# Optimization experiments

Hardware: AMD Instinct MI355X
Metric: run time of the kernel (lower is better)

## Reference

```python
import jax, jax.numpy as jnp
import numpy as np

# NOTE: ffn(in, out, capacity=1, activation) is assumed to be a single Linear(in, out)
# followed by the activation (ReLU). Dropout is identity in eval mode.

B, M, H, Eh = 16, 128, 256, 128

def setup_inputs() -> dict:
    key = jax.random.key(0)
    ks = jax.random.split(key, 12)
    s = lambda n: 1.0 / np.sqrt(n)
    return {
        "X": jax.random.normal(ks[0], (B, M, H), jnp.float32),
        "E": jax.random.normal(ks[1], (B, M, M, Eh), jnp.float32),
        "A": jax.random.uniform(ks[2], (B, M, M), jnp.float32),
        "eps": jnp.zeros((1,), jnp.float32),
        "We": jax.random.normal(ks[3], (Eh, Eh), jnp.float32) * s(Eh),
        "be": jnp.zeros((Eh,), jnp.float32),
        "Wr": jax.random.normal(ks[4], (H + Eh, H), jnp.float32) * s(H + Eh),
        "br": jnp.zeros((H,), jnp.float32),
        "W0": jax.random.normal(ks[5], (H, H), jnp.float32) * s(H),
        "b0": jnp.zeros((H,), jnp.float32),
        "W1": jax.random.normal(ks[6], (H, H), jnp.float32) * s(H),
        "b1": jnp.zeros((H,), jnp.float32),
    }

def reference(X, E, A, eps, We, be, Wr, br, W0, b0, W1, b1):
    act = jax.nn.relu
    # edge_mapper: ffn(e, e, capacity=1) -> Linear + activation
    Em = act(jnp.einsum('bije,ef->bijf', E, We) + be)          # (b,m,m,e)
    # msg[b,j,:] = sum_i A[b,i,j] * cat(X[b,i,:], Em[b,i,j,:])
    # fused: avoids materializing the (b,m,m,h+e) intermediate
    msg_x = jnp.einsum('bij,bih->bjh', A, X)                   # (b,m,h)
    msg_e = jnp.einsum('bij,bije->bje', A, Em)                 # (b,m,e)
    msg = jnp.concatenate([msg_x, msg_e], axis=-1)             # (b,m,h+e)
    Xs = (1.0 + eps) * X
    out = Xs + act(jnp.einsum('bmc,ch->bmh', msg, Wr) + br)    # residual_mapping
    out = jnp.einsum('bmh,hk->bmk', out, W0) + b0
    out = act(out)  # dropout p is identity in eval mode
    out = jnp.einsum('bmh,hk->bmk', out, W1) + b1
    out = act(out)
    return out
```

## Files before the change

### kernel.cpp

```cpp
#include <hip/hip_runtime.h>

typedef float        f32x4  __attribute__((ext_vector_type(4)));
typedef __bf16       bf16x8 __attribute__((ext_vector_type(8)));
typedef unsigned int u32x4  __attribute__((ext_vector_type(4)));
typedef unsigned short u16;

#define MFMA16(a,b,c) __builtin_amdgcn_mfma_f32_16x16x32_bf16((a),(b),(c),0,0,0)

typedef __attribute__((address_space(3))) unsigned int       as3_u32;
typedef __attribute__((address_space(1))) const unsigned int as1_u32;
__device__ __forceinline__ void gld16(const float* g, float* l) {
    __builtin_amdgcn_global_load_lds((as1_u32*)g, (as3_u32*)l, 16, 0, 0);
}

__device__ __forceinline__ unsigned bf_rnd(float x) {
    unsigned u = __float_as_uint(x);
    return (u + 0x7FFFu + ((u >> 16) & 1u)) & 0xFFFF0000u;
}
__device__ __forceinline__ void split_bf(float x, unsigned &h, unsigned &l) {
    unsigned hr = bf_rnd(x);
    h = hr >> 16;
    float lo = x - __uint_as_float(hr);
    l = bf_rnd(lo) >> 16;
}
__device__ __forceinline__ void split8q(const f32x4 a, const f32x4 b, bf16x8 &hv, bf16x8 &lv) {
    u32x4 hp, lp;
    #pragma unroll
    for (int i = 0; i < 2; ++i) {
        float x0 = (i ? b : a)[0], x1 = (i ? b : a)[1], x2 = (i ? b : a)[2], x3 = (i ? b : a)[3];
        unsigned h0 = __float_as_uint(x0) & 0xFFFF0000u;
        unsigned h1 = __float_as_uint(x1) & 0xFFFF0000u;
        unsigned h2 = __float_as_uint(x2) & 0xFFFF0000u;
        unsigned h3 = __float_as_uint(x3) & 0xFFFF0000u;
        unsigned l0 = bf_rnd(x0 - __uint_as_float(h0));
        unsigned l1 = bf_rnd(x1 - __uint_as_float(h1));
        unsigned l2 = bf_rnd(x2 - __uint_as_float(h2));
        unsigned l3 = bf_rnd(x3 - __uint_as_float(h3));
        hp[i*2+0] = (h0 >> 16) | h1;  lp[i*2+0] = (l0 >> 16) | l1;
        hp[i*2+1] = (h2 >> 16) | h3;  lp[i*2+1] = (l2 >> 16) | l3;
    }
    hv = __builtin_bit_cast(bf16x8, hp);
    lv = __builtin_bit_cast(bf16x8, lp);
}
__device__ __forceinline__ bf16x8 ld16(const u16* p) {
    return __builtin_bit_cast(bf16x8, *(const u32x4*)p);
}

__global__ __launch_bounds__(256) void k_prep(
    const float* __restrict__ We, const float* __restrict__ Wr,
    const float* __restrict__ W0, const float* __restrict__ W1,
    u16* __restrict__ WeTh, u16* __restrict__ WeTl,
    u16* __restrict__ WrTh, u16* __restrict__ WrTl,
    u16* __restrict__ W0Th, u16* __restrict__ W0Tl,
    u16* __restrict__ W1Th, u16* __restrict__ W1Tl)
{
    int t = blockIdx.x * 256 + threadIdx.x;
    float v; u16 *dh, *dl; int dst;
    if (t < 16384) {
        int f = t & 127, e = t >> 7;
        v = We[e*128 + f]; dst = f*128 + e; dh = WeTh; dl = WeTl;
    } else if (t < 16384 + 98304) {
        int u = t - 16384; int h = u & 255, k = u >> 8;
        v = Wr[k*256 + h]; dst = h*384 + k; dh = WrTh; dl = WrTl;
    } else if (t < 16384 + 98304 + 65536) {
        int u = t - 16384 - 98304; int h = u & 255, k = u >> 8;
        v = W0[k*256 + h]; dst = h*256 + k; dh = W0Th; dl = W0Tl;
    } else {
        int u = t - 16384 - 98304 - 65536; int h = u & 255, k = u >> 8;
        v = W1[k*256 + h]; dst = h*256 + k; dh = W1Th; dl = W1Tl;
    }
    unsigned hh, ll; split_bf(v, hh, ll);
    dh[dst] = (u16)hh; dl[dst] = (u16)ll;
}

__device__ __forceinline__ void stage_slab(const float* __restrict__ Eslab,
                                           float* buf, int tid) {
    const int w = tid >> 6, l = tid & 63;
    #pragma unroll
    for (int r = 0; r < 8; ++r) {
        const int q   = (r << 2) + w;
        const int row = (q << 1) + (l >> 5);
        const int cof = (((l & 31) ^ (row & 7)) << 4);
        gld16(Eslab + row*128 + (cof >> 2), buf + (q << 8));
    }
}

__global__ __launch_bounds__(256) __attribute__((amdgpu_waves_per_eu(2, 2)))
void k_edge(
    const float* __restrict__ E, const float* __restrict__ A,
    const u16* __restrict__ WeTh, const u16* __restrict__ WeTl,
    const float* __restrict__ be, float* __restrict__ part)
{
    __shared__ __align__(16) float sE[2][64*128];

    const int tid  = threadIdx.x;
    const int lane = tid & 63;
    const int wv   = tid >> 6;
    const int lrow = lane & 15;
    const int lk   = lane >> 4;
    const int wm   = (wv >> 1) << 5;
    const int wn   = (wv & 1)  << 6;
    const int bid  = blockIdx.x;
    const int jh   = bid & 1;
    const int c    = (bid >> 1) & 15;
    const int b    = bid >> 5;
    const int i0   = c << 3;
    const int j0   = jh << 6;

    bf16x8 wh[4][4], wl[4][4];
    #pragma unroll
    for (int n = 0; n < 4; ++n)
        #pragma unroll
        for (int k = 0; k < 4; ++k) {
            const int off = (wn + n*16 + lrow)*128 + k*32 + lk*8;
            wh[n][k] = ld16(WeTh + off);
            wl[n][k] = ld16(WeTl + off);
        }
    float ber[4];
    #pragma unroll
    for (int n = 0; n < 4; ++n) ber[n] = be[wn + n*16 + lrow];

    const float* Eb = E + ((size_t)((b*128 + i0)*128 + j0)) * 128;
    stage_slab(Eb, sE[0], tid);

    f32x4 P[2][4] = {};

    for (int s = 0; s < 8; ++s) {
        __syncthreads();
        if (s < 7)
            stage_slab(Eb + (size_t)(s+1)*16384, sE[(s+1) & 1], tid);

        const char* buf = (const char*)sE[s & 1];
        f32x4 em[2][4] = {};
        #pragma unroll
        for (int k = 0; k < 4; ++k) {
            #pragma unroll
            for (int m = 0; m < 2; ++m) {
                const int jr = wm + m*16 + lrow;
                const int cb = k*128 + lk*32;
                const int sw = (jr & 7) << 4;
                const f32x4 e0 = *(const f32x4*)(buf + jr*512 + ((cb +  0) ^ sw));
                const f32x4 e1 = *(const f32x4*)(buf + jr*512 + ((cb + 16) ^ sw));
                bf16x8 eh, el; split8q(e0, e1, eh, el);
                #pragma unroll
                for (int n = 0; n < 4; ++n) {
                    em[m][n] = MFMA16(eh, wh[n][k], em[m][n]);
                    em[m][n] = MFMA16(eh, wl[n][k], em[m][n]);
                    em[m][n] = MFMA16(el, wh[n][k], em[m][n]);
                }
            }
        }

        const float* Arow = A + (size_t)(b*128 + i0 + s)*128 + j0;
        #pragma unroll
        for (int m = 0; m < 2; ++m) {
            const f32x4 a4 = *(const f32x4*)(Arow + wm + m*16 + lk*4);
            #pragma unroll
            for (int n = 0; n < 4; ++n)
                #pragma unroll
                for (int r = 0; r < 4; ++r) {
                    float v = fmaxf(em[m][n][r] + ber[n], 0.0f);
                    P[m][n][r] += a4[r] * v;
                }
        }
    }

    float* op = part + (size_t)bid * 8192;
    #pragma unroll
    for (int m = 0; m < 2; ++m)
        #pragma unroll
        for (int r = 0; r < 4; ++r) {
            const int j = wm + m*16 + lk*4 + r;
            #pragma unroll
            for (int n = 0; n < 4; ++n)
                op[j*128 + wn + n*16 + lrow] = P[m][n][r];
        }
}

__global__ __launch_bounds__(256) void k_msg(
    const float* __restrict__ A, const float* __restrict__ X,
    const float* __restrict__ part,
    u16* __restrict__ msg_h, u16* __restrict__ msg_l)
{
    const int bid = blockIdx.x;
    const int tid = threadIdx.x;
    __shared__ float sAt[128*8];

    if (bid < 256) {
        const int b = bid >> 4, jt = bid & 15;
        #pragma unroll
        for (int q = 0; q < 4; ++q) {
            const int e   = (q << 8) + tid;
            const int row = jt*8 + (e >> 7);
            const int f   = e & 127;
            const int jhh = row >> 6, rl = row & 63;
            const float* p = part + ((size_t)(b*32 + jhh))*8192 + rl*128 + f;
            float ssum = 0.f;
            #pragma unroll
            for (int cc = 0; cc < 16; ++cc) ssum += p[(size_t)cc*16384];
            unsigned hh, ll; split_bf(ssum, hh, ll);
            const size_t o = (size_t)(b*128 + row)*384 + 256 + f;
            msg_h[o] = (u16)hh; msg_l[o] = (u16)ll;
        }
    } else {
        const int idx = bid - 256;
        const int b = idx >> 4, jt = idx & 15, j0 = jt << 3;
        #pragma unroll
        for (int q = 0; q < 4; ++q) {
            const int e = tid + q*256;
            sAt[e] = A[(size_t)(b*128 + (e >> 3))*128 + j0 + (e & 7)];
        }
        __syncthreads();
        const int h = tid;
        float acc[8] = {};
        const float* Xb = X + (size_t)b*32768 + h;
        #pragma unroll 2
        for (int i = 0; i < 128; ++i) {
            const float x  = Xb[(size_t)i*256];
            const f32x4 a0 = *(const f32x4*)(sAt + i*8);
            const f32x4 a1 = *(const f32x4*)(sAt + i*8 + 4);
            acc[0] += a0[0]*x; acc[1] += a0[1]*x; acc[2] += a0[2]*x; acc[3] += a0[3]*x;
            acc[4] += a1[0]*x; acc[5] += a1[1]*x; acc[6] += a1[2]*x; acc[7] += a1[3]*x;
        }
        #pragma unroll
        for (int jj = 0; jj < 8; ++jj) {
            unsigned hh, ll; split_bf(acc[jj], hh, ll);
            const size_t o = (size_t)(b*128 + j0 + jj)*384 + h;
            msg_h[o] = (u16)hh; msg_l[o] = (u16)ll;
        }
    }
}

template<int KT, bool RES, bool F32OUT>
__global__ __launch_bounds__(256) void k_tail(
    const u16* __restrict__ Ah, const u16* __restrict__ Al,
    const u16* __restrict__ Bh, const u16* __restrict__ Bl,
    const float* __restrict__ bias, const float* __restrict__ res,
    const float* __restrict__ epsp,
    float* __restrict__ outf, u16* __restrict__ oh, u16* __restrict__ ol)
{
    const int tid  = threadIdx.x;
    const int lane = tid & 63;
    const int wid  = tid >> 6;
    const int lrow = lane & 15;
    const int lk   = lane >> 4;
    const int wm   = (wid >> 1) << 4;
    const int wn   = (wid & 1)  << 5;
    const int r0   = blockIdx.x << 5;
    const int h0   = blockIdx.y << 6;

    const int arow = r0 + wm + lrow;
    const u16* pah = Ah + (size_t)arow*KT + lk*8;
    const u16* pal = Al + (size_t)arow*KT + lk*8;
    const int c0 = h0 + wn + lrow;
    const u16* pb0h = Bh + (size_t)c0*KT + lk*8;
    const u16* pb0l = Bl + (size_t)c0*KT + lk*8;
    const u16* pb1h = pb0h + 16*KT;
    const u16* pb1l = pb0l + 16*KT;

    f32x4 P[2] = {};
    #pragma unroll
    for (int ks = 0; ks < KT/32; ++ks) {
        const bf16x8 ah  = ld16(pah  + ks*32);
        const bf16x8 al  = ld16(pal  + ks*32);
        const bf16x8 b0h = ld16(pb0h + ks*32), b0l = ld16(pb0l + ks*32);
        const bf16x8 b1h = ld16(pb1h + ks*32), b1l = ld16(pb1l + ks*32);
        P[0] = MFMA16(ah, b0h, P[0]);
        P[0] = MFMA16(ah, b0l, P[0]);
        P[0] = MFMA16(al, b0h, P[0]);
        P[1] = MFMA16(ah, b1h, P[1]);
        P[1] = MFMA16(ah, b1l, P[1]);
        P[1] = MFMA16(al, b1h, P[1]);
    }

    const float eps = RES ? epsp[0] : 0.f;
    #pragma unroll
    for (int n = 0; n < 2; ++n) {
        const int col = h0 + wn + n*16 + lrow;
        const float bv = bias[col];
        #pragma unroll
        for (int e = 0; e < 4; ++e) {
            const int r = r0 + wm + lk*4 + e;
            float v = fmaxf(P[n][e] + bv, 0.f);
            if (RES) v += (1.f + eps) * res[(size_t)r*256 + col];
            if (F32OUT) {
                outf[(size_t)r*256 + col] = v;
            } else {
                unsigned hh, ll; split_bf(v, hh, ll);
                oh[(size_t)r*256 + col] = (u16)hh;
                ol[(size_t)r*256 + col] = (u16)ll;
            }
        }
    }
}

extern "C" void kernel_launch(void* const* d_in, const int* in_sizes, int n_in,
                              void* d_out, int out_size, void* d_ws, size_t ws_size,
                              hipStream_t stream)
{
    const float* X   = (const float*)d_in[0];
    const float* E   = (const float*)d_in[1];
    const float* A   = (const float*)d_in[2];
    const float* eps = (const float*)d_in[3];
    const float* We  = (const float*)d_in[4];
    const float* be  = (const float*)d_in[5];
    const float* Wr  = (const float*)d_in[6];
    const float* br  = (const float*)d_in[7];
    const float* W0  = (const float*)d_in[8];
    const float* b0  = (const float*)d_in[9];
    const float* W1  = (const float*)d_in[10];
    const float* b1  = (const float*)d_in[11];
    float* out = (float*)d_out;

    u16* w = (u16*)d_ws;
    u16* WeTh = w;              u16* WeTl = WeTh + 16384;
    u16* WrTh = WeTl + 16384;   u16* WrTl = WrTh + 98304;
    u16* W0Th = WrTl + 98304;   u16* W0Tl = W0Th + 65536;
    u16* W1Th = W0Tl + 65536;   u16* W1Tl = W1Th + 65536;
    u16* msg_h = W1Tl + 65536;  u16* msg_l = msg_h + 786432;
    u16* o1h = msg_l + 786432;  u16* o1l = o1h + 524288;
    u16* o2h = o1l + 524288;    u16* o2l = o2h + 524288;
    float* part = (float*)(o2l + 524288);

    k_prep<<<960, 256, 0, stream>>>(We, Wr, W0, W1,
        WeTh, WeTl, WrTh, WrTl, W0Th, W0Tl, W1Th, W1Tl);
    k_edge<<<512, 256, 0, stream>>>(E, A, WeTh, WeTl, be, part);
    k_msg<<<512, 256, 0, stream>>>(A, X, part, msg_h, msg_l);
    k_tail<384, true , false><<<dim3(64,4), 256, 0, stream>>>(
        msg_h, msg_l, WrTh, WrTl, br, X, eps, nullptr, o1h, o1l);
    k_tail<256, false, false><<<dim3(64,4), 256, 0, stream>>>(
        o1h, o1l, W0Th, W0Tl, b0, nullptr, nullptr, nullptr, o2h, o2l);
    k_tail<256, false, true ><<<dim3(64,4), 256, 0, stream>>>(
        o2h, o2l, W1Th, W1Tl, b1, nullptr, nullptr, out, nullptr, nullptr);
}
```

Baseline: 282.4 us.

## Deepen edge-kernel pipeline to four buffers and pre-pack weights in MFMA fragment order

The edge kernel now gives each block 16 i-rows and 32 j-columns instead of 8 by 64. It keeps four 16 KB LDS slabs with three loads in flight, synchronised by explicit vmcnt waits and barriers in place of __syncthreads. It also stages A in LDS and halves the partial-sum reduction in k_msg. Weights are pre-permuted in k_prep into MFMA fragment-contiguous layout so each lane loads one contiguous 16-byte vector in both k_edge and k_tail. The aim is to hide E streaming latency and make weight loads coalesced, at the cost of hand-tuned wait counts that must match the number of outstanding loads.

```diff
diff --git a/kernel.cpp b/kernel.cpp
--- a/kernel.cpp
+++ b/kernel.cpp
@@ -58,16 +58,28 @@
     float v; u16 *dh, *dl; int dst;
     if (t < 16384) {
         int f = t & 127, e = t >> 7;
-        v = We[e*128 + f]; dst = f*128 + e; dh = WeTh; dl = WeTl;
-    } else if (t < 16384 + 98304) {
+        v = We[e*128 + f];
+        int F = ((f>>6)*4 + ((f>>4)&3))*4 + (e>>5);
+        dst = F*512 + (((e>>3)&3)*16 + (f&15))*8 + (e&7);
+        dh = WeTh; dl = WeTl;
+    } else if (t < 114688) {
         int u = t - 16384; int h = u & 255, k = u >> 8;
-        v = Wr[k*256 + h]; dst = h*384 + k; dh = WrTh; dl = WrTl;
-    } else if (t < 16384 + 98304 + 65536) {
-        int u = t - 16384 - 98304; int h = u & 255, k = u >> 8;
-        v = W0[k*256 + h]; dst = h*256 + k; dh = W0Th; dl = W0Tl;
+        v = Wr[k*256 + h];
+        int F = (h>>4)*12 + (k>>5);
+        dst = F*512 + (((k>>3)&3)*16 + (h&15))*8 + (k&7);
+        dh = WrTh; dl = WrTl;
+    } else if (t < 180224) {
+        int u = t - 114688; int h = u & 255, k = u >> 8;
+        v = W0[k*256 + h];
+        int F = (h>>4)*8 + (k>>5);
+        dst = F*512 + (((k>>3)&3)*16 + (h&15))*8 + (k&7);
+        dh = W0Th; dl = W0Tl;
     } else {
-        int u = t - 16384 - 98304 - 65536; int h = u & 255, k = u >> 8;
-        v = W1[k*256 + h]; dst = h*256 + k; dh = W1Th; dl = W1Tl;
+        int u = t - 180224; int h = u & 255, k = u >> 8;
+        v = W1[k*256 + h];
+        int F = (h>>4)*8 + (k>>5);
+        dst = F*512 + (((k>>3)&3)*16 + (h&15))*8 + (k&7);
+        dh = W1Th; dl = W1Tl;
     }
     unsigned hh, ll; split_bf(v, hh, ll);
     dh[dst] = (u16)hh; dl[dst] = (u16)ll;
@@ -77,11 +89,11 @@
                                            float* buf, int tid) {
     const int w = tid >> 6, l = tid & 63;
     #pragma unroll
-    for (int r = 0; r < 8; ++r) {
+    for (int r = 0; r < 4; ++r) {
         const int q   = (r << 2) + w;
         const int row = (q << 1) + (l >> 5);
-        const int cof = (((l & 31) ^ (row & 7)) << 4);
-        gld16(Eslab + row*128 + (cof >> 2), buf + (q << 8));
+        const int c   = ((l & 31) ^ (row & 7)) << 2;
+        gld16(Eslab + row*128 + c, buf + (q << 8));
     }
 }
 
@@ -91,90 +103,104 @@
     const u16* __restrict__ WeTh, const u16* __restrict__ WeTl,
     const float* __restrict__ be, float* __restrict__ part)
 {
-    __shared__ __align__(16) float sE[2][64*128];
+    __shared__ __align__(16) float sEf[4*4096];
+    __shared__ __align__(16) float sA[512];
 
     const int tid  = threadIdx.x;
     const int lane = tid & 63;
     const int wv   = tid >> 6;
     const int lrow = lane & 15;
     const int lk   = lane >> 4;
-    const int wm   = (wv >> 1) << 5;
+    const int wm   = (wv >> 1) << 4;
     const int wn   = (wv & 1)  << 6;
     const int bid  = blockIdx.x;
-    const int jh   = bid & 1;
-    const int c    = (bid >> 1) & 15;
+    const int jh   = bid & 3;
+    const int c    = (bid >> 2) & 7;
     const int b    = bid >> 5;
-    const int i0   = c << 3;
-    const int j0   = jh << 6;
+    const int i0   = c << 4;
+    const int j0   = jh << 5;
+
+    #pragma unroll
+    for (int q = 0; q < 2; ++q) {
+        const int idx = q*256 + tid;
+        sA[idx] = A[(size_t)(b*128 + i0 + (idx >> 5))*128 + j0 + (idx & 31)];
+    }
+    float ber[4];
+    #pragma unroll
+    for (int n = 0; n < 4; ++n) ber[n] = be[wn + n*16 + lrow];
 
     bf16x8 wh[4][4], wl[4][4];
-    #pragma unroll
-    for (int n = 0; n < 4; ++n)
-        #pragma unroll
-        for (int k = 0; k < 4; ++k) {
-            const int off = (wn + n*16 + lrow)*128 + k*32 + lk*8;
-            wh[n][k] = ld16(WeTh + off);
-            wl[n][k] = ld16(WeTl + off);
-        }
-    float ber[4];
-    #pragma unroll
-    for (int n = 0; n < 4; ++n) ber[n] = be[wn + n*16 + lrow];
+    {
+        const int F0 = (wv & 1) * 16;
+        #pragma unroll
+        for (int n = 0; n < 4; ++n)
+            #pragma unroll
+            for (int k = 0; k < 4; ++k) {
+                const int off = (F0 + n*4 + k)*512 + lane*8;
+                wh[n][k] = ld16(WeTh + off);
+                wl[n][k] = ld16(WeTl + off);
+            }
+    }
+    asm volatile("s_waitcnt vmcnt(0) lgkmcnt(0)" ::: "memory");
 
     const float* Eb = E + ((size_t)((b*128 + i0)*128 + j0)) * 128;
-    stage_slab(Eb, sE[0], tid);
-
-    f32x4 P[2][4] = {};
-
-    for (int s = 0; s < 8; ++s) {
-        __syncthreads();
-        if (s < 7)
-            stage_slab(Eb + (size_t)(s+1)*16384, sE[(s+1) & 1], tid);
-
-        const char* buf = (const char*)sE[s & 1];
-        f32x4 em[2][4] = {};
-        #pragma unroll
-        for (int k = 0; k < 4; ++k) {
-            #pragma unroll
-            for (int m = 0; m < 2; ++m) {
-                const int jr = wm + m*16 + lrow;
-                const int cb = k*128 + lk*32;
-                const int sw = (jr & 7) << 4;
-                const f32x4 e0 = *(const f32x4*)(buf + jr*512 + ((cb +  0) ^ sw));
-                const f32x4 e1 = *(const f32x4*)(buf + jr*512 + ((cb + 16) ^ sw));
-                bf16x8 eh, el; split8q(e0, e1, eh, el);
-                #pragma unroll
-                for (int n = 0; n < 4; ++n) {
-                    em[m][n] = MFMA16(eh, wh[n][k], em[m][n]);
-                    em[m][n] = MFMA16(eh, wl[n][k], em[m][n]);
-                    em[m][n] = MFMA16(el, wh[n][k], em[m][n]);
-                }
-            }
-        }
-
-        const float* Arow = A + (size_t)(b*128 + i0 + s)*128 + j0;
-        #pragma unroll
-        for (int m = 0; m < 2; ++m) {
-            const f32x4 a4 = *(const f32x4*)(Arow + wm + m*16 + lk*4);
-            #pragma unroll
-            for (int n = 0; n < 4; ++n)
-                #pragma unroll
-                for (int r = 0; r < 4; ++r) {
-                    float v = fmaxf(em[m][n][r] + ber[n], 0.0f);
-                    P[m][n][r] += a4[r] * v;
-                }
-        }
-    }
-
-    float* op = part + (size_t)bid * 8192;
-    #pragma unroll
-    for (int m = 0; m < 2; ++m)
-        #pragma unroll
-        for (int r = 0; r < 4; ++r) {
-            const int j = wm + m*16 + lk*4 + r;
-            #pragma unroll
-            for (int n = 0; n < 4; ++n)
-                op[j*128 + wn + n*16 + lrow] = P[m][n][r];
-        }
+    stage_slab(Eb,            sEf,          tid);
+    stage_slab(Eb + 16384,    sEf + 4096,   tid);
+    stage_slab(Eb + 2*16384,  sEf + 2*4096, tid);
+
+    f32x4 P[4] = {};
+
+#define EDGE_STEP(S, NWs)                                                    \
+    {                                                                        \
+        asm volatile("s_waitcnt vmcnt(" NWs ")" ::: "memory");               \
+        __builtin_amdgcn_s_barrier();                                        \
+        __builtin_amdgcn_sched_barrier(0);                                   \
+        if ((S) < 13)                                                        \
+            stage_slab(Eb + (size_t)((S)+3)*16384,                           \
+                       sEf + (((S)+3) & 3)*4096, tid);                       \
+        const char* buf = (const char*)(sEf + ((S) & 3)*4096);               \
+        const int jr = wm + lrow;                                            \
+        const int sw = (jr & 7) << 4;                                        \
+        f32x4 em[4] = {};                                                    \
+        _Pragma("unroll")                                                    \
+        for (int k = 0; k < 4; ++k) {                                        \
+            const int cb = k*128 + lk*32;                                    \
+            const f32x4 e0 = *(const f32x4*)(buf + jr*512 + ((cb +  0)^sw)); \
+            const f32x4 e1 = *(const f32x4*)(buf + jr*512 + ((cb + 16)^sw)); \
+            bf16x8 eh, el; split8q(e0, e1, eh, el);                          \
+            _Pragma("unroll")                                                \
+            for (int n = 0; n < 4; ++n) {                                    \
+                em[n] = MFMA16(eh, wh[n][k], em[n]);                         \
+                em[n] = MFMA16(eh, wl[n][k], em[n]);                         \
+                em[n] = MFMA16(el, wh[n][k], em[n]);                         \
+            }                                                                \
+        }                                                                    \
+        const f32x4 a4 = *(const f32x4*)(sA + (S)*32 + wm + lk*4);           \
+        _Pragma("unroll")                                                    \
+        for (int n = 0; n < 4; ++n)                                          \
+            _Pragma("unroll")                                                \
+            for (int r = 0; r < 4; ++r) {                                    \
+                float v = fmaxf(em[n][r] + ber[n], 0.0f);                    \
+                P[n][r] += a4[r] * v;                                        \
+            }                                                                \
+    }
+
+    EDGE_STEP(0,  "8")  EDGE_STEP(1,  "8")  EDGE_STEP(2,  "8")
+    EDGE_STEP(3,  "8")  EDGE_STEP(4,  "8")  EDGE_STEP(5,  "8")
+    EDGE_STEP(6,  "8")  EDGE_STEP(7,  "8")  EDGE_STEP(8,  "8")
+    EDGE_STEP(9,  "8")  EDGE_STEP(10, "8")  EDGE_STEP(11, "8")
+    EDGE_STEP(12, "8")  EDGE_STEP(13, "8")  EDGE_STEP(14, "4")
+    EDGE_STEP(15, "0")
+#undef EDGE_STEP
+
+    float* op = part + (size_t)bid * 4096;
+    #pragma unroll
+    for (int r = 0; r < 4; ++r) {
+        const int j = wm + lk*4 + r;
+        #pragma unroll
+        for (int n = 0; n < 4; ++n)
+            op[j*128 + wn + n*16 + lrow] = P[n][r];
+    }
 }
 
 __global__ __launch_bounds__(256) void k_msg(
@@ -193,11 +219,11 @@
             const int e   = (q << 8) + tid;
             const int row = jt*8 + (e >> 7);
             const int f   = e & 127;
-            const int jhh = row >> 6, rl = row & 63;
-            const float* p = part + ((size_t)(b*32 + jhh))*8192 + rl*128 + f;
+            const float* p = part + ((size_t)b*32 + (row >> 5))*4096
+                                  + (row & 31)*128 + f;
             float ssum = 0.f;
             #pragma unroll
-            for (int cc = 0; cc < 16; ++cc) ssum += p[(size_t)cc*16384];
+            for (int cc = 0; cc < 8; ++cc) ssum += p[(size_t)cc*16384];
             unsigned hh, ll; split_bf(ssum, hh, ll);
             const size_t o = (size_t)(b*128 + row)*384 + 256 + f;
             msg_h[o] = (u16)hh; msg_l[o] = (u16)ll;
@@ -239,6 +265,7 @@
     const float* __restrict__ epsp,
     float* __restrict__ outf, u16* __restrict__ oh, u16* __restrict__ ol)
 {
+    constexpr int NB = KT/32;
     const int tid  = threadIdx.x;
     const int lane = tid & 63;
     const int wid  = tid >> 6;
@@ -252,19 +279,17 @@
     const int arow = r0 + wm + lrow;
     const u16* pah = Ah + (size_t)arow*KT + lk*8;
     const u16* pal = Al + (size_t)arow*KT + lk*8;
-    const int c0 = h0 + wn + lrow;
-    const u16* pb0h = Bh + (size_t)c0*KT + lk*8;
-    const u16* pb0l = Bl + (size_t)c0*KT + lk*8;
-    const u16* pb1h = pb0h + 16*KT;
-    const u16* pb1l = pb0l + 16*KT;
+    const size_t bb = (size_t)((h0 + wn) >> 4) * NB * 512 + lane*8;
+    const u16* pbh = Bh + bb;
+    const u16* pbl = Bl + bb;
 
     f32x4 P[2] = {};
     #pragma unroll
-    for (int ks = 0; ks < KT/32; ++ks) {
-        const bf16x8 ah  = ld16(pah  + ks*32);
-        const bf16x8 al  = ld16(pal  + ks*32);
-        const bf16x8 b0h = ld16(pb0h + ks*32), b0l = ld16(pb0l + ks*32);
-        const bf16x8 b1h = ld16(pb1h + ks*32), b1l = ld16(pb1l + ks*32);
+    for (int ks = 0; ks < NB; ++ks) {
+        const bf16x8 ah  = ld16(pah + ks*32);
+        const bf16x8 al  = ld16(pal + ks*32);
+        const bf16x8 b0h = ld16(pbh + ks*512), b0l = ld16(pbl + ks*512);
+        const bf16x8 b1h = ld16(pbh + (NB + ks)*512), b1l = ld16(pbl + (NB + ks)*512);
         P[0] = MFMA16(ah, b0h, P[0]);
         P[0] = MFMA16(ah, b0l, P[0]);
         P[0] = MFMA16(al, b0h, P[0]);
```

Result: faster. 267.4 us (-5.3%).
